# Performance work log

Measured on AMD Instinct MI355X. Metric: run time of the kernel, lower is better.

## Reference

```python
import jax, jax.numpy as jnp
import numpy as np

B, S, D, H = 16, 512, 1024, 16
DH = D // H  # 64


def setup_inputs() -> dict:
    key = jax.random.key(0)
    kx, kq, kk, kv = jax.random.split(key, 4)
    stdv = 1.0 / np.sqrt(DH)  # reset_param uses 1/sqrt(t.size(1)) = 1/sqrt(head_dim)
    x = jax.random.normal(kx, (B, S, D), dtype=jnp.float32)
    Wq = jax.random.uniform(kq, (H, D, DH), dtype=jnp.float32, minval=-stdv, maxval=stdv)
    Wk = jax.random.uniform(kk, (H, D, DH), dtype=jnp.float32, minval=-stdv, maxval=stdv)
    Wv = jax.random.uniform(kv, (H, D, DH), dtype=jnp.float32, minval=-stdv, maxval=stdv)
    return {"x": x, "Wq": Wq, "Wk": Wk, "Wv": Wv}


def reference(x, Wq, Wk, Wv):
    # x: [B, S, D]; Wq/Wk/Wv: [H, D, DH] (stacked per-head params)
    q = jnp.einsum('bsd,hde->bhse', x, Wq)  # [B,H,S,DH]
    k = jnp.einsum('bsd,hde->bhse', x, Wk)
    v = jnp.einsum('bsd,hde->bhse', x, Wv)
    # NOTE: original scales by sqrt(input_dim), not sqrt(head_dim)
    scale = 1.0 / jnp.sqrt(jnp.float32(D))
    scores = jnp.einsum('bhse,bhte->bhst', q, k) * scale  # [B,H,S,S]
    attn = jax.nn.softmax(scores, axis=-1)
    out = jnp.einsum('bhst,bhte->bhse', attn, v)  # [B,H,S,DH]
    # concat heads along feature dim (head order matches torch cat over loop)
    return out.transpose(0, 2, 1, 3).reshape(x.shape[0], x.shape[1], D)
```

## Files before the change

kernel.cpp:

```cpp
#include <hip/hip_runtime.h>
#include <math.h>

constexpr int B = 16, S = 512, D = 1024, H = 16, DH = 64;
constexpr int BH = B * H;

typedef short bf16x8 __attribute__((ext_vector_type(8)));
typedef float f32x4  __attribute__((ext_vector_type(4)));

__device__ __forceinline__ unsigned short f2bf(float f) {
    unsigned u = __float_as_uint(f);
    u += 0x7fff + ((u >> 16) & 1);
    return (unsigned short)(u >> 16);
}

__global__ __launch_bounds__(256) void convert_x(
    const float* __restrict__ x, unsigned short* __restrict__ xb)
{
    int i = blockIdx.x * 256 + threadIdx.x;
    float4 v = ((const float4*)x)[i];
    ushort4 o;
    o.x = f2bf(v.x); o.y = f2bf(v.y); o.z = f2bf(v.z); o.w = f2bf(v.w);
    ((ushort4*)xb)[i] = o;
}

__global__ __launch_bounds__(256) void convert_w(
    const float* __restrict__ Wq, const float* __restrict__ Wk,
    const float* __restrict__ Wv, unsigned short* __restrict__ WbT)
{
    __shared__ float tile[64][65];
    const int d0 = blockIdx.x * 64;
    const int h = blockIdx.y, m = blockIdx.z;
    const float* W = ((m == 0) ? Wq : (m == 1) ? Wk : Wv) + (size_t)h * D * DH;
    const int t = threadIdx.x;
    {
        int e = t & 63, dr = t >> 6;
        #pragma unroll
        for (int i = 0; i < 16; ++i) {
            int d = dr * 16 + i;
            tile[d][e] = W[(size_t)(d0 + d) * DH + e];
        }
    }
    __syncthreads();
    {
        int d = t & 63, er = t >> 6;
        unsigned short* out = WbT + (size_t)(m * H + h) * DH * D;
        #pragma unroll
        for (int i = 0; i < 16; ++i) {
            int e = er * 16 + i;
            out[(size_t)e * D + d0 + d] = f2bf(tile[d][e]);
        }
    }
}

__global__ __launch_bounds__(256) void qkv_gemm(
    const unsigned short* __restrict__ xb,
    const unsigned short* __restrict__ WbT,
    unsigned short* __restrict__ qkvb)
{
    __shared__ unsigned short As[128 * 64];
    __shared__ unsigned short Bs[128 * 64];

    const int t = threadIdx.x;
    const int w = t >> 6;
    const int wr = w >> 1, wc = w & 1;
    const int L = t & 63;
    const int lane15 = L & 15;
    const int quad = L >> 4;
    const int lrow8 = L >> 3;
    const int lg = L & 7;

    const int r0 = blockIdx.x * 128;
    const int n0 = blockIdx.y * 128;

    f32x4 acc[4][4] = {};

    for (int k0 = 0; k0 < D; k0 += 64) {
        #pragma unroll
        for (int i = 0; i < 4; ++i) {
            int c = w * 4 + i;
            int r = c * 8 + lrow8;
            int gg = lg ^ (r & 7);
            const unsigned short* gp = xb + (size_t)(r0 + r) * D + k0 + gg * 8;
            __builtin_amdgcn_global_load_lds(
                (const __attribute__((address_space(1))) void*)gp,
                (__attribute__((address_space(3))) void*)(As + c * 512),
                16, 0, 0);
            const unsigned short* gq = WbT + (size_t)(n0 + r) * D + k0 + gg * 8;
            __builtin_amdgcn_global_load_lds(
                (const __attribute__((address_space(1))) void*)gq,
                (__attribute__((address_space(3))) void*)(Bs + c * 512),
                16, 0, 0);
        }
        __syncthreads();

        #pragma unroll
        for (int ks = 0; ks < 2; ++ks) {
            int gk = ks * 4 + quad;
            bf16x8 a[4], bb[4];
            #pragma unroll
            for (int rt = 0; rt < 4; ++rt) {
                int ml = wr * 64 + rt * 16 + lane15;
                a[rt] = *(const bf16x8*)(As + ml * 64 + ((gk ^ (ml & 7)) * 8));
            }
            #pragma unroll
            for (int ct = 0; ct < 4; ++ct) {
                int nl = wc * 64 + ct * 16 + lane15;
                bb[ct] = *(const bf16x8*)(Bs + nl * 64 + ((gk ^ (nl & 7)) * 8));
            }
            #pragma unroll
            for (int rt = 0; rt < 4; ++rt)
                #pragma unroll
                for (int ct = 0; ct < 4; ++ct)
                    acc[rt][ct] = __builtin_amdgcn_mfma_f32_16x16x32_bf16(
                        a[rt], bb[ct], acc[rt][ct], 0, 0, 0);
        }
        __syncthreads();
    }

    const int m  = n0 >> 10;
    const int h  = ((n0 >> 6) + wc) & 15;
    const int bb_ = r0 >> 9;
    const int s0 = (r0 & 511) + wr * 64;

    if (m == 2) {
        unsigned short* outv = qkvb + ((size_t)(2 * BH) + (bb_ * H + h)) * (size_t)(S * DH);
        #pragma unroll
        for (int rt = 0; rt < 4; ++rt) {
            int srow = s0 + rt * 16 + quad * 4;
            #pragma unroll
            for (int ct = 0; ct < 4; ++ct) {
                int e = ct * 16 + lane15;
                ushort4 pk;
                pk.x = f2bf(acc[rt][ct][0]);
                pk.y = f2bf(acc[rt][ct][1]);
                pk.z = f2bf(acc[rt][ct][2]);
                pk.w = f2bf(acc[rt][ct][3]);
                *(ushort4*)(outv + (size_t)e * S + srow) = pk;
            }
        }
    } else {
        const float sc = (m == 0) ? 0.04508422002778011f : 1.0f;
        unsigned short* out = qkvb + ((size_t)m * BH + (bb_ * H + h)) * (size_t)(S * DH);
        #pragma unroll
        for (int rt = 0; rt < 4; ++rt) {
            #pragma unroll
            for (int ct = 0; ct < 4; ++ct) {
                int e = ct * 16 + lane15;
                #pragma unroll
                for (int r = 0; r < 4; ++r) {
                    int srow = s0 + rt * 16 + quad * 4 + r;
                    out[(size_t)srow * DH + e] = f2bf(acc[rt][ct][r] * sc);
                }
            }
        }
    }
}

__global__ __launch_bounds__(256) void attn_mfma(
    const unsigned short* __restrict__ qkvb, float* __restrict__ out)
{
    __shared__ unsigned short Qs[128 * 64];
    __shared__ unsigned short Ks[64 * 64];
    __shared__ unsigned short Vt[64 * 64];

    const int t = threadIdx.x;
    const int w = t >> 6;
    const int L = t & 63;
    const int lane15 = L & 15;
    const int quad = L >> 4;
    const int lrow8 = L >> 3;
    const int lg = L & 7;
    const int qr0 = blockIdx.x * 128;
    const int bh = blockIdx.y;
    const int b = bh >> 4, h = bh & 15;

    const unsigned short* qb = qkvb + (size_t)bh * S * DH;
    const unsigned short* kb = qkvb + (size_t)(BH + bh) * S * DH;
    const unsigned short* vt = qkvb + (size_t)(2 * BH + bh) * S * DH;

    #pragma unroll
    for (int i = 0; i < 4; ++i) {
        int base = w * 32 + i * 8;
        int r = base + lrow8;
        int gg = lg ^ (r & 7);
        const unsigned short* gp = qb + (size_t)(qr0 + r) * DH + gg * 8;
        __builtin_amdgcn_global_load_lds(
            (const __attribute__((address_space(1))) void*)gp,
            (__attribute__((address_space(3))) void*)(Qs + base * 64),
            16, 0, 0);
    }

    f32x4 o[2][4] = {};
    float plsum[2] = {0.f, 0.f};
    bf16x8 qf[2][2];

    for (int kt = 0; kt < S; kt += 64) {
        #pragma unroll
        for (int i = 0; i < 2; ++i) {
            int base = (w * 2 + i) * 8;
            int r = base + lrow8;
            int gr = (r & 32) | ((r & 12) << 1) | ((r & 16) >> 2) | (r & 3);
            int gg = lg ^ (r & 7);
            const unsigned short* gpk = kb + (size_t)(kt + gr) * DH + gg * 8;
            __builtin_amdgcn_global_load_lds(
                (const __attribute__((address_space(1))) void*)gpk,
                (__attribute__((address_space(3))) void*)(Ks + base * 64),
                16, 0, 0);
            const unsigned short* gpv = vt + (size_t)r * S + kt + gg * 8;
            __builtin_amdgcn_global_load_lds(
                (const __attribute__((address_space(1))) void*)gpv,
                (__attribute__((address_space(3))) void*)(Vt + base * 64),
                16, 0, 0);
        }
        __syncthreads();

        if (kt == 0) {
            #pragma unroll
            for (int mt = 0; mt < 2; ++mt)
                #pragma unroll
                for (int ks = 0; ks < 2; ++ks) {
                    int ml = w * 32 + mt * 16 + lane15;
                    int gk = ks * 4 + quad;
                    qf[mt][ks] = *(const bf16x8*)(Qs + ml * 64 + ((gk ^ (lane15 & 7)) * 8));
                }
        }

        f32x4 st[2][4] = {};
        #pragma unroll
        for (int ks = 0; ks < 2; ++ks) {
            int gk = ks * 4 + quad;
            bf16x8 kf[4];
            #pragma unroll
            for (int ct = 0; ct < 4; ++ct) {
                int kr = ct * 16 + lane15;
                kf[ct] = *(const bf16x8*)(Ks + kr * 64 + ((gk ^ (lane15 & 7)) * 8));
            }
            #pragma unroll
            for (int mt = 0; mt < 2; ++mt)
                #pragma unroll
                for (int ct = 0; ct < 4; ++ct)
                    st[mt][ct] = __builtin_amdgcn_mfma_f32_16x16x32_bf16(
                        kf[ct], qf[mt][ks], st[mt][ct], 0, 0, 0);
        }

        bf16x8 pB[2][2];
        #pragma unroll
        for (int mt = 0; mt < 2; ++mt) {
            float rs = 0.f;
            #pragma unroll
            for (int ct = 0; ct < 4; ++ct) {
                float p0 = exp2f(st[mt][ct][0]);
                float p1 = exp2f(st[mt][ct][1]);
                float p2 = exp2f(st[mt][ct][2]);
                float p3 = exp2f(st[mt][ct][3]);
                rs += (p0 + p1) + (p2 + p3);
                int hi = (ct & 1) * 4;
                pB[mt][ct >> 1][hi + 0] = (short)f2bf(p0);
                pB[mt][ct >> 1][hi + 1] = (short)f2bf(p1);
                pB[mt][ct >> 1][hi + 2] = (short)f2bf(p2);
                pB[mt][ct >> 1][hi + 3] = (short)f2bf(p3);
            }
            plsum[mt] += rs;
        }

        #pragma unroll
        for (int ks = 0; ks < 2; ++ks) {
            int gk = ks * 4 + quad;
            bf16x8 vf[4];
            #pragma unroll
            for (int nt = 0; nt < 4; ++nt) {
                int dh = nt * 16 + lane15;
                vf[nt] = *(const bf16x8*)(Vt + dh * 64 + ((gk ^ (lane15 & 7)) * 8));
            }
            #pragma unroll
            for (int mt = 0; mt < 2; ++mt)
                #pragma unroll
                for (int nt = 0; nt < 4; ++nt)
                    o[mt][nt] = __builtin_amdgcn_mfma_f32_16x16x32_bf16(
                        vf[nt], pB[mt][ks], o[mt][nt], 0, 0, 0);
        }
        __syncthreads();
    }

    #pragma unroll
    for (int mt = 0; mt < 2; ++mt) {
        float l = plsum[mt];
        l += __shfl_xor(l, 16, 64);
        l += __shfl_xor(l, 32, 64);
        float inv = 1.0f / l;
        int srow = qr0 + w * 32 + mt * 16 + lane15;
        float* op = out + (size_t)(b * S + srow) * D + h * DH;
        #pragma unroll
        for (int nt = 0; nt < 4; ++nt) {
            float4 v;
            v.x = o[mt][nt][0] * inv;
            v.y = o[mt][nt][1] * inv;
            v.z = o[mt][nt][2] * inv;
            v.w = o[mt][nt][3] * inv;
            *(float4*)(op + nt * 16 + quad * 4) = v;
        }
    }
}

extern "C" void kernel_launch(void* const* d_in, const int* in_sizes, int n_in,
                              void* d_out, int out_size, void* d_ws, size_t ws_size,
                              hipStream_t stream) {
    const float* x  = (const float*)d_in[0];
    const float* Wq = (const float*)d_in[1];
    const float* Wk = (const float*)d_in[2];
    const float* Wv = (const float*)d_in[3];
    float* outp = (float*)d_out;

    unsigned short* qkvb = (unsigned short*)d_ws;
    unsigned short* xb   = (unsigned short*)((char*)d_ws + 50331648);
    unsigned short* WbT  = (unsigned short*)((char*)d_ws + 67108864);

    convert_x<<<dim3((B * S * D / 4) / 256), 256, 0, stream>>>(x, xb);
    convert_w<<<dim3(D / 64, H, 3), 256, 0, stream>>>(Wq, Wk, Wv, WbT);
    qkv_gemm<<<dim3(B * S / 128, 3 * H * DH / 128), 256, 0, stream>>>(xb, WbT, qkvb);
    attn_mfma<<<dim3(S / 128, BH), 256, 0, stream>>>(qkvb, outp);
}
```

Baseline: 196.7 us.

## Rewrite QKV GEMM as 256x256 tile with double-buffered async LDS pipeline

The QKV projection GEMM moves from 128x128 tiles with 4 waves to 256x256 tiles with 8 waves, and each wave now computes a 128x64 sub-tile. Global-to-LDS loads are double-buffered and issued in halves, interleaved between MFMA phases with explicit vmcnt waits, barriers and setprio. The goal is to hide load latency and raise data reuse per tile. In exchange it needs much more LDS (128 KB) and more accumulator registers, and it launches fewer blocks.

After: 214.7 us. +9.1%, slower.

```diff
diff --git a/kernel.cpp b/kernel.cpp
--- a/kernel.cpp
+++ b/kernel.cpp
@@ -52,89 +52,197 @@
     }
 }
 
-__global__ __launch_bounds__(256) void qkv_gemm(
+#define VMC8  asm volatile("s_waitcnt vmcnt(8)" ::: "memory")
+#define VMC4  asm volatile("s_waitcnt vmcnt(4)" ::: "memory")
+#define VMC0  asm volatile("s_waitcnt vmcnt(0)" ::: "memory")
+#define LGKM0 asm volatile("s_waitcnt lgkmcnt(0)" ::: "memory")
+#define BARR  __builtin_amdgcn_s_barrier()
+
+__device__ __forceinline__ void stage_half(
+    const unsigned short* __restrict__ src, int grow0, int k0,
+    unsigned short* dst, int t)
+{
+    #pragma unroll
+    for (int r = 0; r < 2; ++r) {
+        int row = r * 64 + (t >> 3);
+        int gg = (t & 7) ^ (row & 7);
+        __builtin_amdgcn_global_load_lds(
+            (const __attribute__((address_space(1))) void*)
+                (src + (size_t)(grow0 + row) * 1024 + k0 + gg * 8),
+            (__attribute__((address_space(3))) void*)(dst + r * 4096 + t * 8),
+            16, 0, 0);
+    }
+}
+
+template<int MODE>
+__device__ __forceinline__ void kiter(
+    const unsigned short* __restrict__ xb,
+    const unsigned short* __restrict__ WbT,
+    unsigned short* As0, unsigned short* Bs0,
+    f32x4 (&acc)[8][4], int kb,
+    int r0, int n0, int t, int wr, int wc, int lane15, int quad)
+{
+    #pragma unroll
+    for (int half = 0; half < 2; ++half) {
+        const unsigned short* Ab = As0 + half * 16384;
+        const unsigned short* Bb = Bs0 + half * 16384;
+        unsigned short* AsT = half ? As0 + 16384 : As0;
+        unsigned short* BsT = half ? Bs0 : Bs0 + 16384;
+        const int arow = wr * 128, brow = wc * 64;
+        const int kB = kb + (1 + half) * 64;
+        const int kA = kb + (2 + half) * 64;
+        const bool doB = !(MODE == 0 && half == 0) && !(MODE == 2 && half == 1);
+        const bool doA = (MODE != 2);
+
+        bf16x8 a0[4][2], a1[4][2], b0[2][2], b1[2][2];
+
+        #pragma unroll
+        for (int mt = 0; mt < 4; ++mt)
+            #pragma unroll
+            for (int ks = 0; ks < 2; ++ks) {
+                int rl = arow + mt * 16 + lane15, gk = ks * 4 + quad;
+                a0[mt][ks] = *(const bf16x8*)(Ab + rl * 64 + (gk ^ (rl & 7)) * 8);
+            }
+        #pragma unroll
+        for (int nt = 0; nt < 2; ++nt)
+            #pragma unroll
+            for (int ks = 0; ks < 2; ++ks) {
+                int rl = brow + nt * 16 + lane15, gk = ks * 4 + quad;
+                b0[nt][ks] = *(const bf16x8*)(Bb + rl * 64 + (gk ^ (rl & 7)) * 8);
+            }
+        if (doB) stage_half(WbT, n0, kB, BsT, t);
+        BARR; LGKM0;
+        __builtin_amdgcn_s_setprio(1);
+        #pragma unroll
+        for (int mt = 0; mt < 4; ++mt)
+            #pragma unroll
+            for (int nt = 0; nt < 2; ++nt) {
+                acc[mt][nt] = __builtin_amdgcn_mfma_f32_16x16x32_bf16(
+                    a0[mt][0], b0[nt][0], acc[mt][nt], 0, 0, 0);
+                acc[mt][nt] = __builtin_amdgcn_mfma_f32_16x16x32_bf16(
+                    a0[mt][1], b0[nt][1], acc[mt][nt], 0, 0, 0);
+            }
+        __builtin_amdgcn_s_setprio(0);
+        BARR;
+
+        #pragma unroll
+        for (int mt = 0; mt < 4; ++mt)
+            #pragma unroll
+            for (int ks = 0; ks < 2; ++ks) {
+                int rl = arow + 64 + mt * 16 + lane15, gk = ks * 4 + quad;
+                a1[mt][ks] = *(const bf16x8*)(Ab + rl * 64 + (gk ^ (rl & 7)) * 8);
+            }
+        if (doB) stage_half(WbT, n0 + 128, kB, BsT + 8192, t);
+        BARR; LGKM0;
+        __builtin_amdgcn_s_setprio(1);
+        #pragma unroll
+        for (int mt = 0; mt < 4; ++mt)
+            #pragma unroll
+            for (int nt = 0; nt < 2; ++nt) {
+                acc[4 + mt][nt] = __builtin_amdgcn_mfma_f32_16x16x32_bf16(
+                    a1[mt][0], b0[nt][0], acc[4 + mt][nt], 0, 0, 0);
+                acc[4 + mt][nt] = __builtin_amdgcn_mfma_f32_16x16x32_bf16(
+                    a1[mt][1], b0[nt][1], acc[4 + mt][nt], 0, 0, 0);
+            }
+        __builtin_amdgcn_s_setprio(0);
+        BARR;
+
+        #pragma unroll
+        for (int j = 0; j < 2; ++j)
+            #pragma unroll
+            for (int ks = 0; ks < 2; ++ks) {
+                int rl = brow + 32 + j * 16 + lane15, gk = ks * 4 + quad;
+                b1[j][ks] = *(const bf16x8*)(Bb + rl * 64 + (gk ^ (rl & 7)) * 8);
+            }
+        if (doA) stage_half(xb, r0, kA, AsT, t);
+        BARR; LGKM0;
+        __builtin_amdgcn_s_setprio(1);
+        #pragma unroll
+        for (int mt = 0; mt < 4; ++mt)
+            #pragma unroll
+            for (int j = 0; j < 2; ++j) {
+                acc[4 + mt][2 + j] = __builtin_amdgcn_mfma_f32_16x16x32_bf16(
+                    a1[mt][0], b1[j][0], acc[4 + mt][2 + j], 0, 0, 0);
+                acc[4 + mt][2 + j] = __builtin_amdgcn_mfma_f32_16x16x32_bf16(
+                    a1[mt][1], b1[j][1], acc[4 + mt][2 + j], 0, 0, 0);
+            }
+        __builtin_amdgcn_s_setprio(0);
+        BARR;
+
+        if (doA) stage_half(xb, r0 + 128, kA, AsT + 8192, t);
+        BARR; LGKM0;
+        __builtin_amdgcn_s_setprio(1);
+        #pragma unroll
+        for (int mt = 0; mt < 4; ++mt)
+            #pragma unroll
+            for (int j = 0; j < 2; ++j) {
+                acc[mt][2 + j] = __builtin_amdgcn_mfma_f32_16x16x32_bf16(
+                    a0[mt][0], b1[j][0], acc[mt][2 + j], 0, 0, 0);
+                acc[mt][2 + j] = __builtin_amdgcn_mfma_f32_16x16x32_bf16(
+                    a0[mt][1], b1[j][1], acc[mt][2 + j], 0, 0, 0);
+            }
+        __builtin_amdgcn_s_setprio(0);
+        if (half == 0) { if (MODE == 2) { VMC0; } else { VMC4; } }
+        else           { if (MODE != 2) { VMC4; } }
+        BARR;
+    }
+}
+
+__global__ __launch_bounds__(512, 2) void qkv_gemm(
     const unsigned short* __restrict__ xb,
     const unsigned short* __restrict__ WbT,
     unsigned short* __restrict__ qkvb)
 {
-    __shared__ unsigned short As[128 * 64];
-    __shared__ unsigned short Bs[128 * 64];
+    __shared__ unsigned short As[2 * 16384];
+    __shared__ unsigned short Bs[2 * 16384];
 
     const int t = threadIdx.x;
     const int w = t >> 6;
-    const int wr = w >> 1, wc = w & 1;
+    const int wr = w >> 2, wc = w & 3;
     const int L = t & 63;
     const int lane15 = L & 15;
     const int quad = L >> 4;
-    const int lrow8 = L >> 3;
-    const int lg = L & 7;
-
-    const int r0 = blockIdx.x * 128;
-    const int n0 = blockIdx.y * 128;
-
-    f32x4 acc[4][4] = {};
-
-    for (int k0 = 0; k0 < D; k0 += 64) {
-        #pragma unroll
-        for (int i = 0; i < 4; ++i) {
-            int c = w * 4 + i;
-            int r = c * 8 + lrow8;
-            int gg = lg ^ (r & 7);
-            const unsigned short* gp = xb + (size_t)(r0 + r) * D + k0 + gg * 8;
-            __builtin_amdgcn_global_load_lds(
-                (const __attribute__((address_space(1))) void*)gp,
-                (__attribute__((address_space(3))) void*)(As + c * 512),
-                16, 0, 0);
-            const unsigned short* gq = WbT + (size_t)(n0 + r) * D + k0 + gg * 8;
-            __builtin_amdgcn_global_load_lds(
-                (const __attribute__((address_space(1))) void*)gq,
-                (__attribute__((address_space(3))) void*)(Bs + c * 512),
-                16, 0, 0);
-        }
-        __syncthreads();
-
-        #pragma unroll
-        for (int ks = 0; ks < 2; ++ks) {
-            int gk = ks * 4 + quad;
-            bf16x8 a[4], bb[4];
-            #pragma unroll
-            for (int rt = 0; rt < 4; ++rt) {
-                int ml = wr * 64 + rt * 16 + lane15;
-                a[rt] = *(const bf16x8*)(As + ml * 64 + ((gk ^ (ml & 7)) * 8));
-            }
-            #pragma unroll
-            for (int ct = 0; ct < 4; ++ct) {
-                int nl = wc * 64 + ct * 16 + lane15;
-                bb[ct] = *(const bf16x8*)(Bs + nl * 64 + ((gk ^ (nl & 7)) * 8));
-            }
-            #pragma unroll
-            for (int rt = 0; rt < 4; ++rt)
-                #pragma unroll
-                for (int ct = 0; ct < 4; ++ct)
-                    acc[rt][ct] = __builtin_amdgcn_mfma_f32_16x16x32_bf16(
-                        a[rt], bb[ct], acc[rt][ct], 0, 0, 0);
-        }
-        __syncthreads();
-    }
+
+    const int r0 = blockIdx.x * 256;
+    const int n0 = blockIdx.y * 256;
+
+    f32x4 acc[8][4] = {};
+
+    stage_half(xb,  r0,       0,  As,                t);
+    stage_half(xb,  r0 + 128, 0,  As + 8192,         t);
+    stage_half(WbT, n0,       0,  Bs,                t);
+    stage_half(WbT, n0 + 128, 0,  Bs + 8192,         t);
+    stage_half(xb,  r0,       64, As + 16384,        t);
+    stage_half(xb,  r0 + 128, 64, As + 16384 + 8192, t);
+    stage_half(WbT, n0,       64, Bs + 16384,        t);
+    stage_half(WbT, n0 + 128, 64, Bs + 16384 + 8192, t);
+    VMC8;
+    BARR;
+
+    kiter<0>(xb, WbT, As, Bs, acc, 0, r0, n0, t, wr, wc, lane15, quad);
+    #pragma unroll 1
+    for (int it = 1; it < 7; ++it)
+        kiter<1>(xb, WbT, As, Bs, acc, it * 128, r0, n0, t, wr, wc, lane15, quad);
+    kiter<2>(xb, WbT, As, Bs, acc, 896, r0, n0, t, wr, wc, lane15, quad);
 
     const int m  = n0 >> 10;
     const int h  = ((n0 >> 6) + wc) & 15;
     const int bb_ = r0 >> 9;
-    const int s0 = (r0 & 511) + wr * 64;
+    const int s0 = (r0 & 511) + wr * 128;
 
     if (m == 2) {
         unsigned short* outv = qkvb + ((size_t)(2 * BH) + (bb_ * H + h)) * (size_t)(S * DH);
         #pragma unroll
-        for (int rt = 0; rt < 4; ++rt) {
-            int srow = s0 + rt * 16 + quad * 4;
-            #pragma unroll
-            for (int ct = 0; ct < 4; ++ct) {
-                int e = ct * 16 + lane15;
+        for (int mt = 0; mt < 8; ++mt) {
+            int srow = s0 + mt * 16 + quad * 4;
+            #pragma unroll
+            for (int nt = 0; nt < 4; ++nt) {
+                int e = nt * 16 + lane15;
                 ushort4 pk;
-                pk.x = f2bf(acc[rt][ct][0]);
-                pk.y = f2bf(acc[rt][ct][1]);
-                pk.z = f2bf(acc[rt][ct][2]);
-                pk.w = f2bf(acc[rt][ct][3]);
+                pk.x = f2bf(acc[mt][nt][0]);
+                pk.y = f2bf(acc[mt][nt][1]);
+                pk.z = f2bf(acc[mt][nt][2]);
+                pk.w = f2bf(acc[mt][nt][3]);
                 *(ushort4*)(outv + (size_t)e * S + srow) = pk;
             }
         }
@@ -142,14 +250,14 @@
         const float sc = (m == 0) ? 0.04508422002778011f : 1.0f;
         unsigned short* out = qkvb + ((size_t)m * BH + (bb_ * H + h)) * (size_t)(S * DH);
         #pragma unroll
-        for (int rt = 0; rt < 4; ++rt) {
-            #pragma unroll
-            for (int ct = 0; ct < 4; ++ct) {
-                int e = ct * 16 + lane15;
+        for (int mt = 0; mt < 8; ++mt) {
+            #pragma unroll
+            for (int nt = 0; nt < 4; ++nt) {
+                int e = nt * 16 + lane15;
                 #pragma unroll
                 for (int r = 0; r < 4; ++r) {
-                    int srow = s0 + rt * 16 + quad * 4 + r;
-                    out[(size_t)srow * DH + e] = f2bf(acc[rt][ct][r] * sc);
+                    int srow = s0 + mt * 16 + quad * 4 + r;
+                    out[(size_t)srow * DH + e] = f2bf(acc[mt][nt][r] * sc);
                 }
             }
         }
@@ -317,6 +425,6 @@
 
     convert_x<<<dim3((B * S * D / 4) / 256), 256, 0, stream>>>(x, xb);
     convert_w<<<dim3(D / 64, H, 3), 256, 0, stream>>>(Wq, Wk, Wv, WbT);
-    qkv_gemm<<<dim3(B * S / 128, 3 * H * DH / 128), 256, 0, stream>>>(xb, WbT, qkvb);
+    qkv_gemm<<<dim3(B * S / 256, 3 * H * DH / 256), 512, 0, stream>>>(xb, WbT, qkvb);
     attn_mfma<<<dim3(S / 128, BH), 256, 0, stream>>>(qkvb, outp);
 }
```

## Double-buffer K/V tiles in attention kernel to overlap loads with MFMA

Applied to the files above, without the earlier changes.

Gives the attention kernel two LDS buffers each for K and V, prefetching the next key tile with async global-to-LDS loads while the current tile is computed. The per-iteration pair of __syncthreads becomes a single vmcnt(0) wait plus barrier, and the Q fragment load moves ahead of the loop. It also raises wave priority around the MFMA blocks. The aim is to hide global load latency behind compute, at the cost of 16KB more LDS per block, which may lower occupancy.

After: 196.8 us. About the same (+0.0%).

```diff
diff --git a/kernel.cpp b/kernel.cpp
--- a/kernel.cpp
+++ b/kernel.cpp
@@ -12,6 +12,9 @@
     u += 0x7fff + ((u >> 16) & 1);
     return (unsigned short)(u >> 16);
 }
+
+#define VMC0  asm volatile("s_waitcnt vmcnt(0)" ::: "memory")
+#define BARR  __builtin_amdgcn_s_barrier()
 
 __global__ __launch_bounds__(256) void convert_x(
     const float* __restrict__ x, unsigned short* __restrict__ xb)
@@ -156,12 +159,35 @@
     }
 }
 
+__device__ __forceinline__ void stage_kv(
+    const unsigned short* __restrict__ kb, const unsigned short* __restrict__ vt,
+    int kt, unsigned short* Kd, unsigned short* Vd, int w, int lrow8, int lg)
+{
+    #pragma unroll
+    for (int i = 0; i < 2; ++i) {
+        int base = (w * 2 + i) * 8;
+        int r = base + lrow8;
+        int gr = (r & 32) | ((r & 12) << 1) | ((r & 16) >> 2) | (r & 3);
+        int gg = lg ^ (r & 7);
+        __builtin_amdgcn_global_load_lds(
+            (const __attribute__((address_space(1))) void*)
+                (kb + (size_t)(kt + gr) * DH + gg * 8),
+            (__attribute__((address_space(3))) void*)(Kd + base * 64),
+            16, 0, 0);
+        __builtin_amdgcn_global_load_lds(
+            (const __attribute__((address_space(1))) void*)
+                (vt + (size_t)r * S + kt + gg * 8),
+            (__attribute__((address_space(3))) void*)(Vd + base * 64),
+            16, 0, 0);
+    }
+}
+
 __global__ __launch_bounds__(256) void attn_mfma(
     const unsigned short* __restrict__ qkvb, float* __restrict__ out)
 {
     __shared__ unsigned short Qs[128 * 64];
-    __shared__ unsigned short Ks[64 * 64];
-    __shared__ unsigned short Vt[64 * 64];
+    __shared__ unsigned short Ks[2][64 * 64];
+    __shared__ unsigned short Vt[2][64 * 64];
 
     const int t = threadIdx.x;
     const int w = t >> 6;
@@ -189,41 +215,30 @@
             (__attribute__((address_space(3))) void*)(Qs + base * 64),
             16, 0, 0);
     }
+    stage_kv(kb, vt, 0, &Ks[0][0], &Vt[0][0], w, lrow8, lg);
+    VMC0;
+    BARR;
+
+    bf16x8 qf[2][2];
+    #pragma unroll
+    for (int mt = 0; mt < 2; ++mt)
+        #pragma unroll
+        for (int ks = 0; ks < 2; ++ks) {
+            int ml = w * 32 + mt * 16 + lane15;
+            int gk = ks * 4 + quad;
+            qf[mt][ks] = *(const bf16x8*)(Qs + ml * 64 + ((gk ^ (lane15 & 7)) * 8));
+        }
 
     f32x4 o[2][4] = {};
     float plsum[2] = {0.f, 0.f};
-    bf16x8 qf[2][2];
-
+
+    #pragma unroll 2
     for (int kt = 0; kt < S; kt += 64) {
-        #pragma unroll
-        for (int i = 0; i < 2; ++i) {
-            int base = (w * 2 + i) * 8;
-            int r = base + lrow8;
-            int gr = (r & 32) | ((r & 12) << 1) | ((r & 16) >> 2) | (r & 3);
-            int gg = lg ^ (r & 7);
-            const unsigned short* gpk = kb + (size_t)(kt + gr) * DH + gg * 8;
-            __builtin_amdgcn_global_load_lds(
-                (const __attribute__((address_space(1))) void*)gpk,
-                (__attribute__((address_space(3))) void*)(Ks + base * 64),
-                16, 0, 0);
-            const unsigned short* gpv = vt + (size_t)r * S + kt + gg * 8;
-            __builtin_amdgcn_global_load_lds(
-                (const __attribute__((address_space(1))) void*)gpv,
-                (__attribute__((address_space(3))) void*)(Vt + base * 64),
-                16, 0, 0);
-        }
-        __syncthreads();
-
-        if (kt == 0) {
-            #pragma unroll
-            for (int mt = 0; mt < 2; ++mt)
-                #pragma unroll
-                for (int ks = 0; ks < 2; ++ks) {
-                    int ml = w * 32 + mt * 16 + lane15;
-                    int gk = ks * 4 + quad;
-                    qf[mt][ks] = *(const bf16x8*)(Qs + ml * 64 + ((gk ^ (lane15 & 7)) * 8));
-                }
-        }
+        const int cur = (kt >> 6) & 1;
+        const int nxt = cur ^ 1;
+
+        if (kt + 64 < S)
+            stage_kv(kb, vt, kt + 64, &Ks[nxt][0], &Vt[nxt][0], w, lrow8, lg);
 
         f32x4 st[2][4] = {};
         #pragma unroll
@@ -233,14 +248,16 @@
             #pragma unroll
             for (int ct = 0; ct < 4; ++ct) {
                 int kr = ct * 16 + lane15;
-                kf[ct] = *(const bf16x8*)(Ks + kr * 64 + ((gk ^ (lane15 & 7)) * 8));
-            }
+                kf[ct] = *(const bf16x8*)(&Ks[cur][0] + kr * 64 + ((gk ^ (lane15 & 7)) * 8));
+            }
+            __builtin_amdgcn_s_setprio(1);
             #pragma unroll
             for (int mt = 0; mt < 2; ++mt)
                 #pragma unroll
                 for (int ct = 0; ct < 4; ++ct)
                     st[mt][ct] = __builtin_amdgcn_mfma_f32_16x16x32_bf16(
                         kf[ct], qf[mt][ks], st[mt][ct], 0, 0, 0);
+            __builtin_amdgcn_s_setprio(0);
         }
 
         bf16x8 pB[2][2];
@@ -270,16 +287,20 @@
             #pragma unroll
             for (int nt = 0; nt < 4; ++nt) {
                 int dh = nt * 16 + lane15;
-                vf[nt] = *(const bf16x8*)(Vt + dh * 64 + ((gk ^ (lane15 & 7)) * 8));
-            }
+                vf[nt] = *(const bf16x8*)(&Vt[cur][0] + dh * 64 + ((gk ^ (lane15 & 7)) * 8));
+            }
+            __builtin_amdgcn_s_setprio(1);
             #pragma unroll
             for (int mt = 0; mt < 2; ++mt)
                 #pragma unroll
                 for (int nt = 0; nt < 4; ++nt)
                     o[mt][nt] = __builtin_amdgcn_mfma_f32_16x16x32_bf16(
                         vf[nt], pB[mt][ks], o[mt][nt], 0, 0, 0);
-        }
-        __syncthreads();
+            __builtin_amdgcn_s_setprio(0);
+        }
+
+        VMC0;
+        BARR;
     }
 
     #pragma unroll
```
